# Performance work log

Hardware: AMD Instinct MI355X
Metric: run time of the kernel (lower is better)

The kernel has to match this reference:

```python
import jax, jax.numpy as jnp
import numpy as np

N, T = 32, 1500
ENC_DIM, DEC_DIM = 1024, 1024
ATT_DIM, ATT_HEAD = 512, 4
HA = ATT_DIM * ATT_HEAD


def setup_inputs() -> dict:
    key = jax.random.key(0)
    ks = jax.random.split(key, 12)
    enc_pad = jax.random.normal(ks[0], (N, T, ENC_DIM), dtype=jnp.float32)
    enc_len = jax.random.randint(ks[1], (N,), T // 2, T + 1)
    enc_len = enc_len.at[0].set(T)  # ensure max == T (original code assumes mask width == T)
    dec_prev = jax.random.normal(ks[2], (N, DEC_DIM), dtype=jnp.float32)
    ali_prev = jnp.zeros((N, T), dtype=jnp.float32)  # unused by forward
    s = 0.02
    W_enc = jax.random.normal(ks[3], (ENC_DIM, HA), dtype=jnp.float32) * s
    b_enc = jnp.zeros((HA,), dtype=jnp.float32)
    W_key = jax.random.normal(ks[4], (ENC_DIM, HA), dtype=jnp.float32) * s
    W_dec = jax.random.normal(ks[5], (DEC_DIM, HA), dtype=jnp.float32) * s
    W_ctx = jax.random.normal(ks[6], (HA, ENC_DIM), dtype=jnp.float32) * s
    b_ctx = jnp.zeros((ENC_DIM,), dtype=jnp.float32)
    # grouped Conv1d(HA -> H, kernel=1, groups=H, bias=False): weight [H, A]
    w_conv = jax.random.normal(ks[7], (ATT_HEAD, ATT_DIM), dtype=jnp.float32) * s
    return dict(enc_pad=enc_pad, enc_len=enc_len, dec_prev=dec_prev, ali_prev=ali_prev,
                W_enc=W_enc, b_enc=b_enc, W_key=W_key, W_dec=W_dec,
                W_ctx=W_ctx, b_ctx=b_ctx, w_conv=w_conv)


def reference(enc_pad, enc_len, dec_prev, ali_prev,
              W_enc, b_enc, W_key, W_dec, W_ctx, b_ctx, w_conv):
    n, t, _ = enc_pad.shape
    H, A = ATT_HEAD, ATT_DIM
    # enc_part: N x H x T x A
    enc_part = (enc_pad @ W_enc + b_enc).reshape(n, t, H, A).transpose(0, 2, 1, 3)
    # key_part: N x H x A x T
    key_part = (enc_pad @ W_key).reshape(n, t, H, A).transpose(0, 2, 3, 1)
    # dec_part: N x H x A
    dec_part = (dec_prev @ W_dec).reshape(n, H, A)
    # additive score: tanh(key + dec), grouped 1x1 conv scorer -> N x H x T
    sum_part = jnp.tanh(key_part + dec_part[:, :, :, None])
    e = jnp.einsum('nhat,ha->nht', sum_part, w_conv)
    # padding mask: True where t >= enc_len
    pad_mask = jnp.arange(t)[None, :] >= enc_len[:, None]  # N x T
    e = jnp.where(pad_mask[:, None, :], -jnp.inf, e)
    ali = jax.nn.softmax(e, axis=-1)  # N x H x T
    # weighted sum over time, then context projection
    ctx = jnp.einsum('nht,nhta->nha', ali, enc_part).reshape(n, H * A)
    ctx = ctx @ W_ctx + b_ctx  # N x D_enc
    return ali, ctx
```

## Files before the change

kernel.cpp:

```cpp
#include <hip/hip_runtime.h>
#include <hip/hip_bf16.h>


#define N_B   32
#define T_S   1500
#define ENC_D 1024
#define HA_D  2048
#define A_D   512
#define H_N   4
#define MROWS 48000

typedef short s8v  __attribute__((ext_vector_type(8)));
typedef float f32x4 __attribute__((ext_vector_type(4)));

__device__ __forceinline__ unsigned short f2bf(float f) {
    unsigned u = __float_as_uint(f);
    unsigned r = (u + 0x7FFFu + ((u >> 16) & 1u)) >> 16;
    return (unsigned short)r;
}
__device__ __forceinline__ float bf2f(unsigned short b) {
    return __uint_as_float(((unsigned)b) << 16);
}
__device__ __forceinline__ float fast_tanh(float x) {
    float e2 = __expf(2.0f * x);
    return 1.0f - __fdividef(2.0f, e2 + 1.0f);
}
__device__ __forceinline__ void gload_lds16(const void* g, void* l) {
    __builtin_amdgcn_global_load_lds(
        (const unsigned int __attribute__((address_space(1)))*)g,
        (unsigned int __attribute__((address_space(3)))*)l, 16, 0, 0);
}

__device__ __forceinline__ void skinny_body(
    int bid, const float* __restrict__ X, const float* __restrict__ W,
    const float* __restrict__ bias, float* __restrict__ Y,
    int Ncols, int ct_mask, int ct_shift, int xA, int xB, float* xT ) {
    const int tid = threadIdx.x;
    const int ct = bid & ct_mask, ks = bid >> ct_shift;
    const int c0 = ct << 8, k0 = ks << 6;
    const int hsel = c0 >> 9;
    {
        const int n = tid >> 3, kk0 = (tid & 7) << 3;
        const float* xr = X + (size_t)n * xA + hsel * xB + k0 + kk0;
        float4 v0 = *(const float4*)xr;
        float4 v1 = *(const float4*)(xr + 4);
        xT[(kk0 + 0) * 36 + n] = v0.x;
        xT[(kk0 + 1) * 36 + n] = v0.y;
        xT[(kk0 + 2) * 36 + n] = v0.z;
        xT[(kk0 + 3) * 36 + n] = v0.w;
        xT[(kk0 + 4) * 36 + n] = v1.x;
        xT[(kk0 + 5) * 36 + n] = v1.y;
        xT[(kk0 + 6) * 36 + n] = v1.z;
        xT[(kk0 + 7) * 36 + n] = v1.w;
    }
    __syncthreads();
    const int w = tid >> 6, lane = tid & 63;
    f32x4 acc[8];
    if (bias != nullptr && ks == 0) {
        f32x4 bv = *(const f32x4*)&bias[c0 + (lane << 2)];
#pragma unroll
        for (int j = 0; j < 8; ++j) acc[j] = bv;
    } else {
#pragma unroll
        for (int j = 0; j < 8; ++j) { f32x4 z = {0.f, 0.f, 0.f, 0.f}; acc[j] = z; }
    }
    const float* Wp = W + (size_t)k0 * Ncols + c0 + (lane << 2);
#pragma unroll 4
    for (int kk = 0; kk < 64; ++kk) {
        f32x4 wf = *(const f32x4*)(Wp + (size_t)kk * Ncols);
        f32x4 xlo = *(const f32x4*)&xT[kk * 36 + w * 8];
        f32x4 xhi = *(const f32x4*)&xT[kk * 36 + w * 8 + 4];
#pragma unroll
        for (int j = 0; j < 4; ++j) {
            acc[j]     += xlo[j] * wf;
            acc[4 + j] += xhi[j] * wf;
        }
    }
#pragma unroll
    for (int j = 0; j < 8; ++j) {
        float* yp = Y + (size_t)(w * 8 + j) * Ncols + c0 + (lane << 2);
#pragma unroll
        for (int i = 0; i < 4; ++i) atomicAdd(yp + i, acc[j][i]);
    }
}

__global__ __launch_bounds__(256) void skinny_k(
    const float* __restrict__ X, const float* __restrict__ W,
    const float* __restrict__ bias, float* __restrict__ Y,
    int Ncols, int ct_mask, int ct_shift, int xA, int xB) {
    __shared__ float xT[64 * 36];
    skinny_body(blockIdx.x, X, W, bias, Y, Ncols, ct_mask, ct_shift, xA, xB, xT);
}

__global__ __launch_bounds__(256) void prep_k(
    const float* __restrict__ enc_pad, const float* __restrict__ Wk,
    const float* __restrict__ dec_prev, const float* __restrict__ W_dec,
    const int* __restrict__ enc_len,
    unsigned short* __restrict__ Xb, unsigned short* __restrict__ Wt,
    float* __restrict__ dp) {
    __shared__ float shmem[64 * 65];
    const int b = blockIdx.x;
    const int tid = threadIdx.x;
    if (b < 128) {
        skinny_body(b, dec_prev, W_dec, nullptr, dp, HA_D, 7, 3, 1024, 0, shmem);
    } else if (b < 640) {
        float (*ld)[65] = (float(*)[65])shmem;
        const int bb = b - 128;
        const int tx = tid & 63, ty = tid >> 6;
        const int c0 = (bb & 31) * 64, d0 = (bb >> 5) * 64;
#pragma unroll
        for (int j = 0; j < 16; ++j)
            ld[ty + 4 * j][tx] = Wk[(size_t)(d0 + ty + 4 * j) * HA_D + c0 + tx];
        __syncthreads();
#pragma unroll
        for (int j = 0; j < 16; ++j)
            Wt[(size_t)(c0 + ty + 4 * j) * ENC_D + d0 + tx] = f2bf(ld[tx][ty + 4 * j]);
    } else {
        const int cb = b - 640;
        const int n = cb / 94, tch = cb - n * 94;
        const int t0 = tch * 16;
        if (t0 >= enc_len[n]) return;
        const int rmax = (1500 - t0 < 16) ? (1500 - t0) : 16;
        const float4* in = (const float4*)enc_pad + ((size_t)n * 1500 + t0) * 256;
        ushort4* out = (ushort4*)Xb + ((size_t)n * 1500 + t0) * 256;
#pragma unroll
        for (int it = 0; it < 16; ++it) {
            int j = it * 256 + tid;
            if ((j >> 8) < rmax) {
                float4 v = in[j];
                ushort4 o;
                o.x = f2bf(v.x); o.y = f2bf(v.y); o.z = f2bf(v.z); o.w = f2bf(v.w);
                out[j] = o;
            }
        }
    }
}

__global__ __launch_bounds__(512) void fused_score_k(
    const unsigned short* __restrict__ Xb, const unsigned short* __restrict__ Wt,
    const float* __restrict__ dec, const float* __restrict__ wconv,
    const int* __restrict__ enc_len, float* __restrict__ e_out) {
    __shared__ unsigned short As[128 * 64];
    __shared__ unsigned short Bs[256 * 64];
    __shared__ float e_s[128];

    const int tid = threadIdx.x;
    const int lane = tid & 63, wid = tid >> 6;
    const int wr = wid >> 2, wc = wid & 3;
    const int l15 = lane & 15, lhi = lane >> 4;

    int orig = blockIdx.x;
    int wgid = (orig & 7) * 375 + (orig >> 3);
    const int mtile = wgid >> 3, nt = wgid & 7;
    const int r0 = mtile * 128;
    const int bcol0 = nt * 256;
    const int h = nt >> 1;

    {
        int n0 = (int)((unsigned)r0 / 1500u);
        int t0 = r0 - n0 * 1500;
        if (t0 + 127 < 1500 && t0 >= enc_len[n0]) return;
    }

    if (tid < 128) e_s[tid] = 0.f;

    const unsigned short* aSrc[2]; int aDst[2];
#pragma unroll
    for (int ld = 0; ld < 2; ++ld) {
        int li = ld * 512 + tid, rowL = li >> 3, c16 = li & 7;
        aSrc[ld] = Xb + (size_t)(r0 + rowL) * ENC_D + ((c16 ^ (rowL & 7)) << 3);
        aDst[ld] = li * 8;
    }
    const unsigned short* bSrc[4]; int bDst[4];
#pragma unroll
    for (int ld = 0; ld < 4; ++ld) {
        int li = ld * 512 + tid, colL = li >> 3, c16 = li & 7;
        bSrc[ld] = Wt + (size_t)(bcol0 + colL) * ENC_D + ((c16 ^ (colL & 7)) << 3);
        bDst[ld] = li * 8;
    }

    const int cA0 = (lhi * 8) ^ ((l15 & 7) << 3);
    const int cA1 = (32 + lhi * 8) ^ ((l15 & 7) << 3);
    const int arow = wr * 64 + l15;
    const int bcol = wc * 64 + l15;

    f32x4 acc[4][4];
#pragma unroll
    for (int m = 0; m < 4; ++m)
#pragma unroll
        for (int n2 = 0; n2 < 4; ++n2) {
            f32x4 z = {0.f, 0.f, 0.f, 0.f};
            acc[m][n2] = z;
        }

    for (int ks = 0; ks < 16; ++ks) {
        const int kb = ks << 6;
#pragma unroll
        for (int ld = 0; ld < 2; ++ld) gload_lds16(aSrc[ld] + kb, As + aDst[ld]);
#pragma unroll
        for (int ld = 0; ld < 4; ++ld) gload_lds16(bSrc[ld] + kb, Bs + bDst[ld]);
        __syncthreads();
#pragma unroll
        for (int kk = 0; kk < 2; ++kk) {
            const int cc = kk ? cA1 : cA0;
            s8v af[4], bv[4];
#pragma unroll
            for (int m = 0; m < 4; ++m)
                af[m] = *(const s8v*)&As[(arow + m * 16) * 64 + cc];
#pragma unroll
            for (int n2 = 0; n2 < 4; ++n2)
                bv[n2] = *(const s8v*)&Bs[(bcol + n2 * 16) * 64 + cc];
#pragma unroll
            for (int m = 0; m < 4; ++m)
#pragma unroll
                for (int n2 = 0; n2 < 4; ++n2)
                    acc[m][n2] = __builtin_amdgcn_mfma_f32_16x16x32_bf16(af[m], bv[n2], acc[m][n2], 0, 0, 0);
        }
        __syncthreads();
    }

    float wv[4];
#pragma unroll
    for (int n2 = 0; n2 < 4; ++n2)
        wv[n2] = wconv[bcol0 + wc * 64 + n2 * 16 + l15];
#pragma unroll
    for (int m = 0; m < 4; ++m) {
#pragma unroll
        for (int rg = 0; rg < 4; ++rg) {
            int row_l = wr * 64 + m * 16 + lhi * 4 + rg;
            int grow = r0 + row_l;
            int nn = (int)((unsigned)grow / 1500u);
            const float* dsl = dec + (size_t)nn * HA_D + bcol0 + wc * 64 + l15;
            float s = 0.f;
#pragma unroll
            for (int n2 = 0; n2 < 4; ++n2) {
                float v = acc[m][n2][rg] + dsl[n2 * 16];
                s += wv[n2] * fast_tanh(v);
            }
            s += __shfl_xor(s, 1); s += __shfl_xor(s, 2);
            s += __shfl_xor(s, 4); s += __shfl_xor(s, 8);
            if (l15 == 0) atomicAdd(&e_s[row_l], s);
        }
    }
    __syncthreads();
    if (tid < 128) {
        int grow = r0 + tid;
        int nn = grow / 1500, tt = grow - nn * 1500;
        atomicAdd(&e_out[(size_t)(nn * H_N + h) * T_S + tt], e_s[tid]);
    }
}

__global__ __launch_bounds__(256) void sm_wenc_k(
    const unsigned short* __restrict__ Xb, const float* __restrict__ e,
    const int* __restrict__ enc_len, float* __restrict__ ali,
    float* __restrict__ ctx_zero, float* __restrict__ wenc) {
    const int b = blockIdx.x, tid = threadIdx.x;
    const int lane = tid & 63, wv = tid >> 6;
    __shared__ float mzs[4][2];
    __shared__ float ps[4][94];
    __shared__ float red[4];
    if (b < 512) {
        const int n = b >> 4, tq = b & 15;
        const int len = enc_len[n];
        const int t0 = tq * 94;
        if (t0 >= len) return;
        const int tcnt = (t0 + 94 <= T_S) ? 94 : (T_S - t0);
        {
            const float* erow = e + (size_t)(n * H_N + wv) * T_S;
            float ev[24];
            float mx = -__builtin_inff();
#pragma unroll
            for (int i = 0; i < 24; ++i) {
                int t = lane + i * 64;
                float v = (t < len) ? erow[t] : -__builtin_inff();
                ev[i] = v;
                mx = fmaxf(mx, v);
            }
#pragma unroll
            for (int o = 32; o; o >>= 1) mx = fmaxf(mx, __shfl_xor(mx, o));
            float Z = 0.f;
#pragma unroll
            for (int i = 0; i < 24; ++i) Z += __expf(ev[i] - mx);
#pragma unroll
            for (int o = 32; o; o >>= 1) Z += __shfl_xor(Z, o);
            if (lane == 0) { mzs[wv][0] = mx; mzs[wv][1] = 1.0f / Z; }
        }
        __syncthreads();
#pragma unroll
        for (int i = 0; i < 2; ++i) {
            int idx = tid + i * 256;
            if (idx < 376) {
                int hh = idx / 94, tt = idx - hh * 94;
                int t = t0 + tt;
                float v = 0.f;
                if (t < len)
                    v = __expf(e[(size_t)(n * H_N + hh) * T_S + t] - mzs[hh][0]) * mzs[hh][1];
                ps[hh][tt] = v;
            }
        }
        __syncthreads();
        const int d0 = tid * 4;
        float a[4][4] = {};
        const unsigned short* xp = Xb + (size_t)(n * T_S + t0) * ENC_D + d0;
#pragma unroll 4
        for (int t = 0; t < tcnt; ++t) {
            ushort4 xv = *(const ushort4*)&xp[(size_t)t * ENC_D];
            float x0 = bf2f(xv.x), x1 = bf2f(xv.y), x2 = bf2f(xv.z), x3 = bf2f(xv.w);
#pragma unroll
            for (int hh = 0; hh < 4; ++hh) {
                float al = ps[hh][t];
                a[hh][0] = fmaf(al, x0, a[hh][0]);
                a[hh][1] = fmaf(al, x1, a[hh][1]);
                a[hh][2] = fmaf(al, x2, a[hh][2]);
                a[hh][3] = fmaf(al, x3, a[hh][3]);
            }
        }
#pragma unroll
        for (int hh = 0; hh < 4; ++hh)
#pragma unroll
            for (int j = 0; j < 4; ++j)
                atomicAdd(&wenc[(size_t)(n * H_N + hh) * ENC_D + d0 + j], a[hh][j]);
    } else {
        const int bb = b - 512;
        ctx_zero[bb * 256 + tid] = 0.f;
        const int n = bb >> 2;
        const int len = enc_len[n];
        const float* row = e + (size_t)bb * T_S;
        float* orow = ali + (size_t)bb * T_S;
        float p[6];
        float mx = -__builtin_inff();
#pragma unroll
        for (int i = 0; i < 6; ++i) {
            int t = tid + i * 256;
            float v = -__builtin_inff();
            if (t < T_S && t < len) v = row[t];
            p[i] = v;
            mx = fmaxf(mx, v);
        }
#pragma unroll
        for (int o = 32; o; o >>= 1) mx = fmaxf(mx, __shfl_xor(mx, o));
        if (lane == 0) red[wv] = mx;
        __syncthreads();
        mx = fmaxf(fmaxf(red[0], red[1]), fmaxf(red[2], red[3]));
        __syncthreads();
        float sum = 0.f;
#pragma unroll
        for (int i = 0; i < 6; ++i) {
            float qv = (p[i] == -__builtin_inff()) ? 0.f : __expf(p[i] - mx);
            p[i] = qv;
            sum += qv;
        }
#pragma unroll
        for (int o = 32; o; o >>= 1) sum += __shfl_xor(sum, o);
        if (lane == 0) red[wv] = sum;
        __syncthreads();
        sum = red[0] + red[1] + red[2] + red[3];
        float inv = 1.0f / sum;
#pragma unroll
        for (int i = 0; i < 6; ++i) {
            int t = tid + i * 256;
            if (t < T_S) orow[t] = p[i] * inv;
        }
    }
}

extern "C" void kernel_launch(void* const* d_in, const int* in_sizes, int n_in,
                              void* d_out, int out_size, void* d_ws, size_t ws_size,
                              hipStream_t stream) {
    const float* enc_pad  = (const float*)d_in[0];
    const int*   enc_len  = (const int*)d_in[1];
    const float* dec_prev = (const float*)d_in[2];
    const float* W_enc    = (const float*)d_in[4];
    const float* b_enc    = (const float*)d_in[5];
    const float* W_key    = (const float*)d_in[6];
    const float* W_dec    = (const float*)d_in[7];
    const float* W_ctx    = (const float*)d_in[8];
    const float* b_ctx    = (const float*)d_in[9];
    const float* w_conv   = (const float*)d_in[10];

    char* ws = (char*)d_ws;
    unsigned short* Xb = (unsigned short*)ws;
    unsigned short* Wt = (unsigned short*)(ws + 98304000);
    float* dp   = (float*)(ws + 102498304);
    float* e    = (float*)(ws + 102760448);
    float* wenc = (float*)(ws + 103528448);
    float* cpre = (float*)(ws + 104052736);

    float* ali = (float*)d_out;
    float* ctx = ((float*)d_out) + 192000;

    hipMemsetAsync(ws + 102498304, 0, 1816576, stream);
    prep_k<<<3648, 256, 0, stream>>>(enc_pad, W_key, dec_prev, W_dec, enc_len, Xb, Wt, dp);
    fused_score_k<<<3000, 512, 0, stream>>>(Xb, Wt, dp, w_conv, enc_len, e);
    sm_wenc_k<<<640, 256, 0, stream>>>(Xb, e, enc_len, ali, ctx, wenc);
    skinny_k<<<128, 256, 0, stream>>>(wenc, W_enc, b_enc, cpre, HA_D, 7, 3, 4096, 1024);
    skinny_k<<<128, 256, 0, stream>>>(cpre, W_ctx, b_ctx, ctx, ENC_D, 3, 2, 2048, 0);
}
```

Baseline: 362.6 us.

## Fuse fp32-to-bf16 encoder conversion into score GEMM A-tile loads

Removes the separate pass that converts enc_pad to a bf16 workspace copy. The score GEMM now loads fp32 rows directly, packs them to bf16 with v_cvt_pk_bf16_f32 and stores them into swizzled LDS, and the weighted-sum kernel reads fp32 encoder rows. This drops one full read/write of the large encoder tensor. The trade-off is more bytes per A-tile load, repeated across the eight column tiles, and the loss of asynchronous global-to-LDS loads for A in the GEMM.

```diff
diff --git a/kernel.cpp b/kernel.cpp
--- a/kernel.cpp
+++ b/kernel.cpp
@@ -18,8 +18,10 @@
     unsigned r = (u + 0x7FFFu + ((u >> 16) & 1u)) >> 16;
     return (unsigned short)r;
 }
-__device__ __forceinline__ float bf2f(unsigned short b) {
-    return __uint_as_float(((unsigned)b) << 16);
+__device__ __forceinline__ unsigned pk2(float x, float y) {
+    unsigned r;
+    asm("v_cvt_pk_bf16_f32 %0, %1, %2" : "=v"(r) : "v"(x), "v"(y));
+    return r;
 }
 __device__ __forceinline__ float fast_tanh(float x) {
     float e2 = __expf(2.0f * x);
@@ -93,17 +95,15 @@
 }
 
 __global__ __launch_bounds__(256) void prep_k(
-    const float* __restrict__ enc_pad, const float* __restrict__ Wk,
-    const float* __restrict__ dec_prev, const float* __restrict__ W_dec,
-    const int* __restrict__ enc_len,
-    unsigned short* __restrict__ Xb, unsigned short* __restrict__ Wt,
+    const float* __restrict__ Wk, const float* __restrict__ dec_prev,
+    const float* __restrict__ W_dec, unsigned short* __restrict__ Wt,
     float* __restrict__ dp) {
     __shared__ float shmem[64 * 65];
     const int b = blockIdx.x;
     const int tid = threadIdx.x;
     if (b < 128) {
         skinny_body(b, dec_prev, W_dec, nullptr, dp, HA_D, 7, 3, 1024, 0, shmem);
-    } else if (b < 640) {
+    } else {
         float (*ld)[65] = (float(*)[65])shmem;
         const int bb = b - 128;
         const int tx = tid & 63, ty = tid >> 6;
@@ -115,29 +115,11 @@
 #pragma unroll
         for (int j = 0; j < 16; ++j)
             Wt[(size_t)(c0 + ty + 4 * j) * ENC_D + d0 + tx] = f2bf(ld[tx][ty + 4 * j]);
-    } else {
-        const int cb = b - 640;
-        const int n = cb / 94, tch = cb - n * 94;
-        const int t0 = tch * 16;
-        if (t0 >= enc_len[n]) return;
-        const int rmax = (1500 - t0 < 16) ? (1500 - t0) : 16;
-        const float4* in = (const float4*)enc_pad + ((size_t)n * 1500 + t0) * 256;
-        ushort4* out = (ushort4*)Xb + ((size_t)n * 1500 + t0) * 256;
-#pragma unroll
-        for (int it = 0; it < 16; ++it) {
-            int j = it * 256 + tid;
-            if ((j >> 8) < rmax) {
-                float4 v = in[j];
-                ushort4 o;
-                o.x = f2bf(v.x); o.y = f2bf(v.y); o.z = f2bf(v.z); o.w = f2bf(v.w);
-                out[j] = o;
-            }
-        }
     }
 }
 
 __global__ __launch_bounds__(512) void fused_score_k(
-    const unsigned short* __restrict__ Xb, const unsigned short* __restrict__ Wt,
+    const float* __restrict__ encp, const unsigned short* __restrict__ Wt,
     const float* __restrict__ dec, const float* __restrict__ wconv,
     const int* __restrict__ enc_len, float* __restrict__ e_out) {
     __shared__ unsigned short As[128 * 64];
@@ -164,13 +146,13 @@
 
     if (tid < 128) e_s[tid] = 0.f;
 
-    const unsigned short* aSrc[2]; int aDst[2];
-#pragma unroll
-    for (int ld = 0; ld < 2; ++ld) {
-        int li = ld * 512 + tid, rowL = li >> 3, c16 = li & 7;
-        aSrc[ld] = Xb + (size_t)(r0 + rowL) * ENC_D + ((c16 ^ (rowL & 7)) << 3);
-        aDst[ld] = li * 8;
-    }
+    const int st_row = tid >> 2;
+    const int g0 = (tid & 3) << 1;
+    const int r7 = st_row & 7;
+    const float* aF0 = encp + (size_t)(r0 + st_row) * ENC_D + ((g0 ^ r7) << 3);
+    const float* aF1 = encp + (size_t)(r0 + st_row) * ENC_D + (((g0 + 1) ^ r7) << 3);
+    unsigned short* aW0 = &As[st_row * 64 + (g0 << 3)];
+
     const unsigned short* bSrc[4]; int bDst[4];
 #pragma unroll
     for (int ld = 0; ld < 4; ++ld) {
@@ -196,9 +178,17 @@
     for (int ks = 0; ks < 16; ++ks) {
         const int kb = ks << 6;
 #pragma unroll
-        for (int ld = 0; ld < 2; ++ld) gload_lds16(aSrc[ld] + kb, As + aDst[ld]);
-#pragma unroll
         for (int ld = 0; ld < 4; ++ld) gload_lds16(bSrc[ld] + kb, Bs + bDst[ld]);
+        {
+            float4 a0 = *(const float4*)(aF0 + kb);
+            float4 a1 = *(const float4*)(aF0 + kb + 4);
+            float4 a2 = *(const float4*)(aF1 + kb);
+            float4 a3 = *(const float4*)(aF1 + kb + 4);
+            uint4 w0 = {pk2(a0.x, a0.y), pk2(a0.z, a0.w), pk2(a1.x, a1.y), pk2(a1.z, a1.w)};
+            uint4 w1 = {pk2(a2.x, a2.y), pk2(a2.z, a2.w), pk2(a3.x, a3.y), pk2(a3.z, a3.w)};
+            *(uint4*)aW0 = w0;
+            *(uint4*)(aW0 + 8) = w1;
+        }
         __syncthreads();
 #pragma unroll
         for (int kk = 0; kk < 2; ++kk) {
@@ -251,7 +241,7 @@
 }
 
 __global__ __launch_bounds__(256) void sm_wenc_k(
-    const unsigned short* __restrict__ Xb, const float* __restrict__ e,
+    const float* __restrict__ encp, const float* __restrict__ e,
     const int* __restrict__ enc_len, float* __restrict__ ali,
     float* __restrict__ ctx_zero, float* __restrict__ wenc) {
     const int b = blockIdx.x, tid = threadIdx.x;
@@ -301,18 +291,17 @@
         __syncthreads();
         const int d0 = tid * 4;
         float a[4][4] = {};
-        const unsigned short* xp = Xb + (size_t)(n * T_S + t0) * ENC_D + d0;
+        const float* xp = encp + (size_t)(n * T_S + t0) * ENC_D + d0;
 #pragma unroll 4
         for (int t = 0; t < tcnt; ++t) {
-            ushort4 xv = *(const ushort4*)&xp[(size_t)t * ENC_D];
-            float x0 = bf2f(xv.x), x1 = bf2f(xv.y), x2 = bf2f(xv.z), x3 = bf2f(xv.w);
+            float4 xv = *(const float4*)&xp[(size_t)t * ENC_D];
 #pragma unroll
             for (int hh = 0; hh < 4; ++hh) {
                 float al = ps[hh][t];
-                a[hh][0] = fmaf(al, x0, a[hh][0]);
-                a[hh][1] = fmaf(al, x1, a[hh][1]);
-                a[hh][2] = fmaf(al, x2, a[hh][2]);
-                a[hh][3] = fmaf(al, x3, a[hh][3]);
+                a[hh][0] = fmaf(al, xv.x, a[hh][0]);
+                a[hh][1] = fmaf(al, xv.y, a[hh][1]);
+                a[hh][2] = fmaf(al, xv.z, a[hh][2]);
+                a[hh][3] = fmaf(al, xv.w, a[hh][3]);
             }
         }
 #pragma unroll
@@ -379,20 +368,19 @@
     const float* w_conv   = (const float*)d_in[10];
 
     char* ws = (char*)d_ws;
-    unsigned short* Xb = (unsigned short*)ws;
-    unsigned short* Wt = (unsigned short*)(ws + 98304000);
-    float* dp   = (float*)(ws + 102498304);
-    float* e    = (float*)(ws + 102760448);
-    float* wenc = (float*)(ws + 103528448);
-    float* cpre = (float*)(ws + 104052736);
+    unsigned short* Wt = (unsigned short*)ws;
+    float* dp   = (float*)(ws + 4194304);
+    float* e    = (float*)(ws + 4456448);
+    float* wenc = (float*)(ws + 5224448);
+    float* cpre = (float*)(ws + 5748736);
 
     float* ali = (float*)d_out;
     float* ctx = ((float*)d_out) + 192000;
 
-    hipMemsetAsync(ws + 102498304, 0, 1816576, stream);
-    prep_k<<<3648, 256, 0, stream>>>(enc_pad, W_key, dec_prev, W_dec, enc_len, Xb, Wt, dp);
-    fused_score_k<<<3000, 512, 0, stream>>>(Xb, Wt, dp, w_conv, enc_len, e);
-    sm_wenc_k<<<640, 256, 0, stream>>>(Xb, e, enc_len, ali, ctx, wenc);
+    hipMemsetAsync(ws + 4194304, 0, 1816576, stream);
+    prep_k<<<640, 256, 0, stream>>>(W_key, dec_prev, W_dec, Wt, dp);
+    fused_score_k<<<3000, 512, 0, stream>>>(enc_pad, Wt, dp, w_conv, enc_len, e);
+    sm_wenc_k<<<640, 256, 0, stream>>>(enc_pad, e, enc_len, ali, ctx, wenc);
     skinny_k<<<128, 256, 0, stream>>>(wenc, W_enc, b_enc, cpre, HA_D, 7, 3, 4096, 1024);
     skinny_k<<<128, 256, 0, stream>>>(cpre, W_ctx, b_ctx, ctx, ENC_D, 3, 2, 2048, 0);
 }
```

New measurement: 392.8 us. 1.08x slower.
